# Optimization experiments

Measured on AMD Instinct MI355X. Metric: run time of the kernel, lower is better.

The kernel has to match this reference:

```python
import jax, jax.numpy as jnp
import numpy as np

H = 4        # no_heads
CH = 32      # per-head hidden (c_hidden)
INF = 1.0e9

def setup_inputs() -> dict:
    key = jax.random.key(0)
    ks = jax.random.split(key, 8)
    B, I, J, C = 1, 256, 256, 128
    s = 0.02
    return {
        "x": jax.random.normal(ks[0], (B, I, J, C), jnp.float32),
        "mask": jnp.ones((B, I, J), jnp.float32),
        "chunk_size": 0,
        "ln_w": jnp.ones((C,), jnp.float32),
        "ln_b": jnp.zeros((C,), jnp.float32),
        "w_tri": jax.random.normal(ks[1], (C, H), jnp.float32) * s,
        "wq": jax.random.normal(ks[2], (C, H * CH), jnp.float32) * s,
        "wk": jax.random.normal(ks[3], (C, H * CH), jnp.float32) * s,
        "wv": jax.random.normal(ks[4], (C, H * CH), jnp.float32) * s,
        "wg": jax.random.normal(ks[5], (C, H * CH), jnp.float32) * s,
        "bg": jnp.zeros((H * CH,), jnp.float32),
        "wo": jax.random.normal(ks[6], (H * CH, C), jnp.float32) * s,
        "bo": jnp.zeros((C,), jnp.float32),
    }

def _layer_norm(x, w, b, eps=1e-5):
    mu = jnp.mean(x, axis=-1, keepdims=True)
    var = jnp.mean(jnp.square(x - mu), axis=-1, keepdims=True)
    return (x - mu) * jax.lax.rsqrt(var + eps) * w + b

def reference(x, mask, chunk_size, ln_w, ln_b, w_tri, wq, wk, wv, wg, bg, wo, bo):
    # starting=True -> no transpose of (I, J)
    B, I, J, C = x.shape
    xn = _layer_norm(x, ln_w, ln_b)                                   # [B,I,J,C]
    # biases
    mask_bias = (INF * (mask - 1.0))[:, :, None, None, :]             # [B,I,1,1,J]
    tri_bias = jnp.einsum("bijc,ch->bhij", xn, w_tri)[:, None]        # [B,1,H,I,J]
    # gated multi-head attention over the J axis (per row I)
    q = (xn @ wq).reshape(B, I, J, H, CH) * (CH ** -0.5)              # [B,I,J,H,CH]
    k = (xn @ wk).reshape(B, I, J, H, CH)
    v = (xn @ wv).reshape(B, I, J, H, CH)
    scores = jnp.einsum("biqhd,bikhd->bihqk", q, k) + mask_bias + tri_bias
    a = jax.nn.softmax(scores, axis=-1)                               # [B,I,H,J,J]
    o = jnp.einsum("bihqk,bikhd->biqhd", a, v)                        # [B,I,J,H,CH]
    g = jax.nn.sigmoid(xn @ wg + bg).reshape(B, I, J, H, CH)
    o = (o * g).reshape(B, I, J, H * CH)
    return o @ wo + bo                                                # [B,I,J,C]
```

## Files before the change

kernel.cpp:

```cpp
#include <hip/hip_runtime.h>
#include <math.h>

#define NI 256
#define NJ 256
#define NC 128
#define NH 4
#define NCH 32
#define LOG2E 1.4426950408889634f

typedef _Float16 f16x8 __attribute__((ext_vector_type(8)));
typedef unsigned short u16x8 __attribute__((ext_vector_type(8)));
typedef unsigned int u32x4 __attribute__((ext_vector_type(4)));
typedef float f32x16 __attribute__((ext_vector_type(16)));

__device__ __forceinline__ unsigned short f2h(float f) {
    return __builtin_bit_cast(unsigned short, (_Float16)f);
}
__device__ __forceinline__ unsigned pkrtz(float a, float b) {
    return __builtin_bit_cast(unsigned, __builtin_amdgcn_cvt_pkrtz(a, b));
}
__device__ __forceinline__ f32x16 fzero16() {
    f32x16 z;
#pragma unroll
    for (int r = 0; r < 16; ++r) z[r] = 0.f;
    return z;
}
__device__ __forceinline__ f32x16 mfma16f(f16x8 a, f16x8 b, f32x16 c) {
    return __builtin_amdgcn_mfma_f32_32x32x16_f16(a, b, c, 0, 0, 0);
}

__global__ __launch_bounds__(256) void convert_weights(
    const float* __restrict__ wq, const float* __restrict__ wk,
    const float* __restrict__ wv, const float* __restrict__ wg,
    const float* __restrict__ wo, const float* __restrict__ w_tri,
    unsigned short* __restrict__ Wt_all, unsigned short* __restrict__ Wto,
    unsigned short* __restrict__ Wtri_pad)
{
    int id = blockIdx.x * 256 + threadIdx.x;
    if (id < 4 * 16384) {
        int m = id >> 14, r = id & 16383;
        int kk = r >> 7, c = r & 127;
        const float* W = (m == 0) ? wq : (m == 1) ? wk : (m == 2) ? wv : wg;
        Wt_all[(m * 128 + c) * 128 + kk] = f2h(W[kk * 128 + c]);
    } else if (id < 5 * 16384) {
        int r = id - 4 * 16384;
        int kk = r >> 7, c = r & 127;
        Wto[c * 128 + kk] = f2h(wo[kk * 128 + c]);
    } else {
        int r = id - 5 * 16384;
        int col = r >> 7, kk = r & 127;
        Wtri_pad[col * 128 + kk] = (col < NH) ? f2h(w_tri[kk * NH + col]) : (unsigned short)0;
    }
}

#define XNP 136
__global__ __launch_bounds__(256, 2) void ln_proj_mfma(
    const float* __restrict__ x, const float* __restrict__ ln_w, const float* __restrict__ ln_b,
    const unsigned short* __restrict__ Wt_all, const unsigned short* __restrict__ Wtri_pad,
    const float* __restrict__ bg,
    unsigned short* __restrict__ q, unsigned short* __restrict__ k,
    unsigned short* __restrict__ v, unsigned short* __restrict__ g,
    float* __restrict__ tri)
{
    __shared__ unsigned short xn[64 * XNP];
    const int tid = threadIdx.x;
    const long tok0 = (long)blockIdx.x * 64;

    const int lane8 = tid & 7;
#pragma unroll
    for (int p = 0; p < 2; ++p) {
        const int t = p * 32 + (tid >> 3);
        const float4* xrow = (const float4*)(x + (tok0 + t) * NC + lane8 * 16);
        float4 xv[4];
        float s = 0.f;
#pragma unroll
        for (int u = 0; u < 4; ++u) {
            xv[u] = xrow[u];
            s += xv[u].x + xv[u].y + xv[u].z + xv[u].w;
        }
#pragma unroll
        for (int off = 4; off; off >>= 1) s += __shfl_down(s, off, 8);
        const float mu = __shfl(s, 0, 8) * (1.f / (float)NC);
        float s2 = 0.f;
#pragma unroll
        for (int u = 0; u < 4; ++u) {
            float dx;
            dx = xv[u].x - mu; s2 += dx * dx;
            dx = xv[u].y - mu; s2 += dx * dx;
            dx = xv[u].z - mu; s2 += dx * dx;
            dx = xv[u].w - mu; s2 += dx * dx;
        }
#pragma unroll
        for (int off = 4; off; off >>= 1) s2 += __shfl_down(s2, off, 8);
        const float rstd = rsqrtf(__shfl(s2, 0, 8) * (1.f / (float)NC) + 1e-5f);
#pragma unroll
        for (int u = 0; u < 4; ++u) {
            const int c = lane8 * 16 + u * 4;
            const float4 lw = *(const float4*)(ln_w + c);
            const float4 lb = *(const float4*)(ln_b + c);
            float o0 = (xv[u].x - mu) * rstd * lw.x + lb.x;
            float o1 = (xv[u].y - mu) * rstd * lw.y + lb.y;
            float o2 = (xv[u].z - mu) * rstd * lw.z + lb.z;
            float o3 = (xv[u].w - mu) * rstd * lw.w + lb.w;
            *(unsigned*)&xn[t * XNP + c]     = pkrtz(o0, o1);
            *(unsigned*)&xn[t * XNP + c + 2] = pkrtz(o2, o3);
        }
    }
    __syncthreads();

    const int w = tid >> 6, L = tid & 63, lh = L >> 5, lc = L & 31;
    f32x16 acc[2][4], accT[2];
#pragma unroll
    for (int mt = 0; mt < 2; ++mt) {
        accT[mt] = fzero16();
#pragma unroll
        for (int nt = 0; nt < 4; ++nt) acc[mt][nt] = fzero16();
    }

#pragma unroll
    for (int k0 = 0; k0 < 8; ++k0) {
        f16x8 a0 = *(const f16x8*)&xn[(lc)      * XNP + k0 * 16 + lh * 8];
        f16x8 a1 = *(const f16x8*)&xn[(32 + lc) * XNP + k0 * 16 + lh * 8];
#pragma unroll
        for (int nt = 0; nt < 4; ++nt) {
            const int ntile = w + 4 * nt;
            f16x8 b = *(const f16x8*)&Wt_all[(ntile * 32 + lc) * 128 + k0 * 16 + lh * 8];
            acc[0][nt] = mfma16f(a0, b, acc[0][nt]);
            acc[1][nt] = mfma16f(a1, b, acc[1][nt]);
        }
        f16x8 bt = *(const f16x8*)&Wtri_pad[lc * 128 + k0 * 16 + lh * 8];
        accT[0] = mfma16f(a0, bt, accT[0]);
        accT[1] = mfma16f(a1, bt, accT[1]);
    }

    const int a_row = (int)(tok0 >> 8);
    const int b0    = (int)(tok0 & 255);
    int rowl[16];
#pragma unroll
    for (int r = 0; r < 16; ++r) rowl[r] = (r & 3) + 8 * (r >> 2) + 4 * lh;

    if (lc < NH) {
        float* tb = tri + ((long)lc * NI + a_row) * NJ + b0;
#pragma unroll
        for (int mt = 0; mt < 2; ++mt)
#pragma unroll
            for (int r = 0; r < 16; ++r)
                tb[mt * 32 + rowl[r]] = accT[mt][r];
    }

    const float bgv = bg[w * 32 + lc];
    const int token = tid >> 2, c8 = (tid & 3) * 8;
#pragma unroll
    for (int m = 0; m < 4; ++m) {
        __syncthreads();
#pragma unroll
        for (int mt = 0; mt < 2; ++mt) {
#pragma unroll
            for (int r = 0; r < 16; ++r) {
                const int row = mt * 32 + rowl[r];
                float val = acc[mt][m][r];
                if (m == 0) val *= 0.25503486f;
                if (m == 3) val = __builtin_amdgcn_rcpf(1.f + __builtin_amdgcn_exp2f(-LOG2E * (val + bgv)));
                xn[row * XNP + w * 32 + lc] = f2h(val);
            }
        }
        __syncthreads();
        unsigned short* O = (m == 0) ? q : (m == 1) ? k : (m == 2) ? v : g;
#pragma unroll
        for (int hh = 0; hh < 4; ++hh) {
            const u16x8 vec = *(const u16x8*)&xn[token * XNP + hh * 32 + c8];
            *(u16x8*)(O + (((long)a_row * NH + hh) * NJ + b0 + token) * NCH + c8) = vec;
        }
    }
}

__global__ __launch_bounds__(64) void swizzle_triT(
    const float* __restrict__ tri, float* __restrict__ tswz)
{
    __shared__ float Ls[32 * 36];
    const int h = blockIdx.x, qt = blockIdx.y, kt = blockIdx.z;
    const int l = threadIdx.x;
#pragma unroll
    for (int rr = 0; rr < 4; ++rr) {
        const int fi = rr * 64 + l;
        const int row = fi >> 3, c4 = fi & 7;
        *(float4*)&Ls[row * 36 + c4 * 4] =
            *(const float4*)(tri + ((long)h * NI + qt * 32 + row) * NJ + kt * 32 + c4 * 4);
    }
    __syncthreads();
    const int lc = l & 31, lhh = l >> 5;
    float* dst = tswz + (((long)(h * 8 + qt) * 8 + kt) * 64 + l) * 16;
    float vals[16];
#pragma unroll
    for (int r = 0; r < 16; ++r)
        vals[r] = LOG2E * Ls[lc * 36 + kt * 0 + (r & 3) + 8 * (r >> 2) + 4 * lhh];
#pragma unroll
    for (int u = 0; u < 4; ++u)
        *(float4*)(dst + u * 4) = make_float4(vals[4*u], vals[4*u+1], vals[4*u+2], vals[4*u+3]);
}

#define KSP 40
#define VTP 264
#define QSP 40
#define GSP 40
__global__ __launch_bounds__(512, 4) void attn_fused(
    const unsigned short* __restrict__ q, const unsigned short* __restrict__ k,
    const unsigned short* __restrict__ v, const unsigned short* __restrict__ g,
    const float* __restrict__ tswz, const float* __restrict__ mask,
    const unsigned short* __restrict__ Wto, const float* __restrict__ bo,
    float* __restrict__ out)
{
    __shared__ char smem[79360];
    unsigned short* Ks = (unsigned short*)(smem);
    unsigned short* Vt = (unsigned short*)(smem + 20480);
    unsigned short* Qs = (unsigned short*)(smem + 37376);
    unsigned short* Gs = (unsigned short*)(smem + 47616);
    float*       maskb = (float*)(smem + 57856);
    float*         mrg = (float*)(smem + 58880);

    const int i = blockIdx.x, qh = blockIdx.y;
    const int tid = threadIdx.x;
    const int w = tid >> 6, L = tid & 63, lh = L >> 5, lc = L & 31;
    const int wq4 = w & 3, ku = w >> 2;
    const int qt = qh * 4 + wq4;
    const int tb0 = ku * 4;

    if (tid < 256) maskb[tid] = (LOG2E * 1.0e9f) * (mask[i * NJ + tid] - 1.0f);

    int rowl[16];
#pragma unroll
    for (int r = 0; r < 16; ++r) rowl[r] = (r & 3) + 8 * (r >> 2) + 4 * lh;

    f32x16 outacc[2];
    outacc[0] = fzero16(); outacc[1] = fzero16();
    float* myMrg = mrg + ((long)wq4 * 64 + L) * 20;

    for (int h = 0; h < NH; ++h) {
        const long base = ((long)i * NH + h) * NJ * NCH;
#pragma unroll
        for (int it = 0; it < 2; ++it) {
            const int idx = it * 512 + tid;
            const int key = idx >> 2, c8 = (idx & 3) * 8;
            *(u16x8*)&Ks[key * KSP + c8] = *(const u16x8*)(k + base + key * NCH + c8);
        }
        {
            const int row = tid >> 2, c8 = (tid & 3) * 8;
            *(u16x8*)&Qs[row * QSP + c8] = *(const u16x8*)(q + base + (qh * 128 + row) * NCH + c8);
            *(u16x8*)&Gs[row * GSP + c8] = *(const u16x8*)(g + base + (qh * 128 + row) * NCH + c8);
        }
        {
            const int key = tid >> 1, hf = tid & 1;
            const u16x8 r0 = *(const u16x8*)(v + base + key * NCH + hf * 16);
            const u16x8 r1 = *(const u16x8*)(v + base + key * NCH + hf * 16 + 8);
#pragma unroll
            for (int u = 0; u < 8; ++u) {
                Vt[(hf * 16 + u)     * VTP + key] = r0[u];
                Vt[(hf * 16 + 8 + u) * VTP + key] = r1[u];
            }
        }
        __syncthreads();

        const f16x8 a0 = *(const f16x8*)&Qs[(wq4 * 32 + lc) * QSP + lh * 8];
        const f16x8 a1 = *(const f16x8*)&Qs[(wq4 * 32 + lc) * QSP + 16 + lh * 8];

        float ls = 0.f;
        f32x16 O = fzero16();

#pragma unroll
        for (int tt = 0; tt < 4; ++tt) {
            const int t = tb0 + tt;
            const float* tv = tswz + (((long)(h * 8 + qt)) * 8 + t) * 1024 + (long)L * 16;
            f32x16 s;
#pragma unroll
            for (int u = 0; u < 4; ++u) {
                const float4 t4 = *(const float4*)(tv + u * 4);
                s[4*u] = t4.x; s[4*u+1] = t4.y; s[4*u+2] = t4.z; s[4*u+3] = t4.w;
            }
            const f16x8 kb0 = *(const f16x8*)&Ks[(t * 32 + lc) * KSP + lh * 8];
            const f16x8 kb1 = *(const f16x8*)&Ks[(t * 32 + lc) * KSP + 16 + lh * 8];
            s = mfma16f(kb0, a0, s);
            s = mfma16f(kb1, a1, s);

            unsigned pk[8];
#pragma unroll
            for (int gg = 0; gg < 4; ++gg) {
                const float4 mb = *(const float4*)&maskb[t * 32 + gg * 8 + 4 * lh];
                const float p0 = __builtin_amdgcn_exp2f(fminf(s[4*gg+0] + mb.x, 15.f));
                const float p1 = __builtin_amdgcn_exp2f(fminf(s[4*gg+1] + mb.y, 15.f));
                const float p2 = __builtin_amdgcn_exp2f(fminf(s[4*gg+2] + mb.z, 15.f));
                const float p3 = __builtin_amdgcn_exp2f(fminf(s[4*gg+3] + mb.w, 15.f));
                ls += (p0 + p1) + (p2 + p3);
                pk[2*gg]   = pkrtz(p0, p1);
                pk[2*gg+1] = pkrtz(p2, p3);
            }
#pragma unroll
            for (int ss = 0; ss < 2; ++ss) {
                const unsigned give0 = lh ? pk[4*ss]   : pk[4*ss+2];
                const unsigned give1 = lh ? pk[4*ss+1] : pk[4*ss+3];
                const unsigned t0 = __shfl_xor(give0, 32);
                const unsigned t1 = __shfl_xor(give1, 32);
                u32x4 bw;
                bw[0] = lh ? t0 : pk[4*ss];
                bw[1] = lh ? t1 : pk[4*ss+1];
                bw[2] = lh ? pk[4*ss+2] : t0;
                bw[3] = lh ? pk[4*ss+3] : t1;
                const f16x8 pb = __builtin_bit_cast(f16x8, bw);
                const f16x8 va = *(const f16x8*)&Vt[lc * VTP + t * 32 + ss * 16 + lh * 8];
                O = mfma16f(va, pb, O);
            }
        }

        if (ku) {
#pragma unroll
            for (int u = 0; u < 4; ++u)
                *(float4*)(myMrg + u * 4) = make_float4(O[4*u], O[4*u+1], O[4*u+2], O[4*u+3]);
            myMrg[16] = ls;
        }
        __syncthreads();
        if (!ku) {
#pragma unroll
            for (int u = 0; u < 4; ++u) {
                const float4 p4 = *(const float4*)(myMrg + u * 4);
                O[4*u] += p4.x; O[4*u+1] += p4.y; O[4*u+2] += p4.z; O[4*u+3] += p4.w;
            }
            ls += myMrg[16];
            ls += __shfl_xor(ls, 32);
            const float rl = __builtin_amdgcn_rcpf(ls);
            unsigned pg[8];
#pragma unroll
            for (int gg = 0; gg < 4; ++gg) {
                const unsigned short* gp = &Gs[(wq4 * 32 + lc) * GSP + gg * 8 + 4 * lh];
                const float o0 = O[4*gg+0] * rl * (float)*(const _Float16*)&gp[0];
                const float o1 = O[4*gg+1] * rl * (float)*(const _Float16*)&gp[1];
                const float o2 = O[4*gg+2] * rl * (float)*(const _Float16*)&gp[2];
                const float o3 = O[4*gg+3] * rl * (float)*(const _Float16*)&gp[3];
                pg[2*gg]   = pkrtz(o0, o1);
                pg[2*gg+1] = pkrtz(o2, o3);
            }
            unsigned obw[8];
#pragma unroll
            for (int ss = 0; ss < 2; ++ss) {
                const unsigned give0 = lh ? pg[4*ss]   : pg[4*ss+2];
                const unsigned give1 = lh ? pg[4*ss+1] : pg[4*ss+3];
                const unsigned t0 = __shfl_xor(give0, 32);
                const unsigned t1 = __shfl_xor(give1, 32);
                obw[4*ss+0] = lh ? t0 : pg[4*ss];
                obw[4*ss+1] = lh ? t1 : pg[4*ss+1];
                obw[4*ss+2] = lh ? pg[4*ss+2] : t0;
                obw[4*ss+3] = lh ? pg[4*ss+3] : t1;
            }
            u32x4 w0, w1;
#pragma unroll
            for (int u = 0; u < 4; ++u) { w0[u] = obw[u]; w1[u] = obw[4+u]; }
            ((u32x4*)myMrg)[0] = w0;
            ((u32x4*)myMrg)[1] = w1;
        }
        __syncthreads();
        {
            const u32x4 b0v = ((const u32x4*)myMrg)[0];
            const u32x4 b1v = ((const u32x4*)myMrg)[1];
#pragma unroll
            for (int ss = 0; ss < 2; ++ss) {
                const f16x8 ogf = __builtin_bit_cast(f16x8, ss ? b1v : b0v);
#pragma unroll
                for (int c2 = 0; c2 < 2; ++c2) {
                    const f16x8 wa = *(const f16x8*)(Wto + ((ku * 2 + c2) * 32 + lc) * NC
                                                     + h * NCH + ss * 16 + lh * 8);
                    outacc[c2] = mfma16f(wa, ogf, outacc[c2]);
                }
            }
        }
    }

    float* outs = (float*)smem;
#pragma unroll
    for (int ph = 0; ph < 2; ++ph) {
        __syncthreads();
        if (ku == ph) {
#pragma unroll
            for (int c2 = 0; c2 < 2; ++c2)
#pragma unroll
                for (int r = 0; r < 16; ++r)
                    outs[(wq4 * 32 + lc) * 68 + c2 * 32 + rowl[r]] = outacc[c2][r];
        }
        __syncthreads();
#pragma unroll
        for (int it = 0; it < 4; ++it) {
            const int fi = it * 512 + tid;
            const int qrow = fi >> 4, c4 = fi & 15;
            const float4 vv = *(const float4*)&outs[qrow * 68 + c4 * 4];
            const float4 b4 = *(const float4*)(bo + ph * 64 + c4 * 4);
            float4 st;
            st.x = vv.x + b4.x; st.y = vv.y + b4.y;
            st.z = vv.z + b4.z; st.w = vv.w + b4.w;
            *(float4*)(out + ((long)i * NJ + qh * 128 + qrow) * NC + ph * 64 + c4 * 4) = st;
        }
    }
}

extern "C" void kernel_launch(void* const* d_in, const int* in_sizes, int n_in,
                              void* d_out, int out_size, void* d_ws, size_t ws_size,
                              hipStream_t stream) {
    const float* x     = (const float*)d_in[0];
    const float* mask  = (const float*)d_in[1];
    const float* ln_w  = (const float*)d_in[3];
    const float* ln_b  = (const float*)d_in[4];
    const float* w_tri = (const float*)d_in[5];
    const float* wq    = (const float*)d_in[6];
    const float* wk    = (const float*)d_in[7];
    const float* wv    = (const float*)d_in[8];
    const float* wg    = (const float*)d_in[9];
    const float* bg    = (const float*)d_in[10];
    const float* wo    = (const float*)d_in[11];
    const float* bo    = (const float*)d_in[12];
    float* out = (float*)d_out;

    char* p = (char*)d_ws;
    const long TOK = (long)NI * NJ;
    const long QB  = TOK * NC * sizeof(unsigned short);
    unsigned short* q  = (unsigned short*)p; p += QB;
    unsigned short* k  = (unsigned short*)p; p += QB;
    unsigned short* v  = (unsigned short*)p; p += QB;
    unsigned short* g  = (unsigned short*)p; p += QB;
    float* tri  = (float*)p; p += (long)NH * NI * NJ * sizeof(float);
    float* tswz = (float*)p; p += (long)NH * NI * NJ * sizeof(float);
    unsigned short* Wt_all   = (unsigned short*)p; p += 4 * 128 * 128 * sizeof(unsigned short);
    unsigned short* Wto      = (unsigned short*)p; p += 128 * 128 * sizeof(unsigned short);
    unsigned short* Wtri_pad = (unsigned short*)p; p += 32 * 128 * sizeof(unsigned short);

    hipLaunchKernelGGL(convert_weights, dim3(336), dim3(256), 0, stream,
                       wq, wk, wv, wg, wo, w_tri, Wt_all, Wto, Wtri_pad);
    hipLaunchKernelGGL(ln_proj_mfma, dim3(TOK / 64), dim3(256), 0, stream,
                       x, ln_w, ln_b, Wt_all, Wtri_pad, bg, q, k, v, g, tri);
    hipLaunchKernelGGL(swizzle_triT, dim3(NH, 8, 8), dim3(64), 0, stream, tri, tswz);
    hipLaunchKernelGGL(attn_fused, dim3(NI, 2), dim3(512), 0, stream,
                       q, k, v, g, tswz, mask, Wto, bo, out);
}
```

Baseline: 181.4 us.

## Store Q/K/V in MFMA fragment layout and drop attention LDS staging

The projection kernel now writes Q, K and V directly in the per-lane MFMA fragment order, 32-token tiles per head, with V pre-transposed. The attention kernel can then load its operands straight from global memory instead of staging K, V^T and Q through shared memory, which removes the LDS transposes and cuts shared memory enough to raise occupancy. The projection kernel moves to 32-token blocks with per-wave transpose buffers, and weight conversion uses tiled LDS transposes. In exchange, K/V fragments are re-read from global/L2 by every wave rather than shared through LDS.

```diff
diff --git a/kernel.cpp b/kernel.cpp
--- a/kernel.cpp
+++ b/kernel.cpp
@@ -36,40 +36,47 @@
     unsigned short* __restrict__ Wt_all, unsigned short* __restrict__ Wto,
     unsigned short* __restrict__ Wtri_pad)
 {
-    int id = blockIdx.x * 256 + threadIdx.x;
-    if (id < 4 * 16384) {
-        int m = id >> 14, r = id & 16383;
-        int kk = r >> 7, c = r & 127;
-        const float* W = (m == 0) ? wq : (m == 1) ? wk : (m == 2) ? wv : wg;
-        Wt_all[(m * 128 + c) * 128 + kk] = f2h(W[kk * 128 + c]);
-    } else if (id < 5 * 16384) {
-        int r = id - 4 * 16384;
-        int kk = r >> 7, c = r & 127;
-        Wto[c * 128 + kk] = f2h(wo[kk * 128 + c]);
+    __shared__ float Ls[32][33];
+    const int b = blockIdx.x;
+    const int tid = threadIdx.x;
+    if (b < 80) {
+        const int m = b >> 4, tile = b & 15, tr = tile >> 2, tc = tile & 3;
+        const float* W = (m == 0) ? wq : (m == 1) ? wk : (m == 2) ? wv : (m == 3) ? wg : wo;
+        const int r = tid >> 3, c4 = (tid & 7) * 4;
+        const float4 v4 = *(const float4*)(W + (tr * 32 + r) * 128 + tc * 32 + c4);
+        Ls[r][c4 + 0] = v4.x; Ls[r][c4 + 1] = v4.y;
+        Ls[r][c4 + 2] = v4.z; Ls[r][c4 + 3] = v4.w;
+        __syncthreads();
+        unsigned short* D = (m < 4) ? (Wt_all + m * 16384) : Wto;
+        ushort4 o;
+        o.x = f2h(Ls[c4 + 0][r]); o.y = f2h(Ls[c4 + 1][r]);
+        o.z = f2h(Ls[c4 + 2][r]); o.w = f2h(Ls[c4 + 3][r]);
+        *(ushort4*)(D + (tc * 32 + r) * 128 + tr * 32 + c4) = o;
     } else {
-        int r = id - 5 * 16384;
-        int col = r >> 7, kk = r & 127;
-        Wtri_pad[col * 128 + kk] = (col < NH) ? f2h(w_tri[kk * NH + col]) : (unsigned short)0;
+        const int kk = tid & 127, c0 = tid >> 7;
+        for (int cc = c0; cc < 32; cc += 2)
+            Wtri_pad[cc * 128 + kk] = (cc < NH) ? f2h(w_tri[kk * NH + cc]) : (unsigned short)0;
     }
 }
 
 #define XNP 136
-__global__ __launch_bounds__(256, 2) void ln_proj_mfma(
+#define TSP 40
+__global__ __launch_bounds__(256, 3) void ln_proj_mfma(
     const float* __restrict__ x, const float* __restrict__ ln_w, const float* __restrict__ ln_b,
     const unsigned short* __restrict__ Wt_all, const unsigned short* __restrict__ Wtri_pad,
     const float* __restrict__ bg,
-    unsigned short* __restrict__ q, unsigned short* __restrict__ k,
-    unsigned short* __restrict__ v, unsigned short* __restrict__ g,
+    unsigned short* __restrict__ q_f, unsigned short* __restrict__ k_f,
+    unsigned short* __restrict__ v_f, unsigned short* __restrict__ g_p,
     float* __restrict__ tri)
 {
-    __shared__ unsigned short xn[64 * XNP];
+    __shared__ unsigned short xn[32 * XNP];
+    __shared__ unsigned short tw[4][32 * TSP];
     const int tid = threadIdx.x;
-    const long tok0 = (long)blockIdx.x * 64;
+    const long tok0 = (long)blockIdx.x * 32;
 
     const int lane8 = tid & 7;
-#pragma unroll
-    for (int p = 0; p < 2; ++p) {
-        const int t = p * 32 + (tid >> 3);
+    const int t = tid >> 3;
+    {
         const float4* xrow = (const float4*)(x + (tok0 + t) * NC + lane8 * 16);
         float4 xv[4];
         float s = 0.f;
@@ -109,67 +116,64 @@
     __syncthreads();
 
     const int w = tid >> 6, L = tid & 63, lh = L >> 5, lc = L & 31;
-    f32x16 acc[2][4], accT[2];
-#pragma unroll
-    for (int mt = 0; mt < 2; ++mt) {
-        accT[mt] = fzero16();
-#pragma unroll
-        for (int nt = 0; nt < 4; ++nt) acc[mt][nt] = fzero16();
-    }
+    f32x16 acc[4], accT;
+#pragma unroll
+    for (int nt = 0; nt < 4; ++nt) acc[nt] = fzero16();
+    accT = fzero16();
 
 #pragma unroll
     for (int k0 = 0; k0 < 8; ++k0) {
-        f16x8 a0 = *(const f16x8*)&xn[(lc)      * XNP + k0 * 16 + lh * 8];
-        f16x8 a1 = *(const f16x8*)&xn[(32 + lc) * XNP + k0 * 16 + lh * 8];
+        const f16x8 a0 = *(const f16x8*)&xn[lc * XNP + k0 * 16 + lh * 8];
 #pragma unroll
         for (int nt = 0; nt < 4; ++nt) {
-            const int ntile = w + 4 * nt;
-            f16x8 b = *(const f16x8*)&Wt_all[(ntile * 32 + lc) * 128 + k0 * 16 + lh * 8];
-            acc[0][nt] = mfma16f(a0, b, acc[0][nt]);
-            acc[1][nt] = mfma16f(a1, b, acc[1][nt]);
-        }
-        f16x8 bt = *(const f16x8*)&Wtri_pad[lc * 128 + k0 * 16 + lh * 8];
-        accT[0] = mfma16f(a0, bt, accT[0]);
-        accT[1] = mfma16f(a1, bt, accT[1]);
-    }
-
-    const int a_row = (int)(tok0 >> 8);
-    const int b0    = (int)(tok0 & 255);
+            const f16x8 b = *(const f16x8*)&Wt_all[((w + 4 * nt) * 32 + lc) * 128 + k0 * 16 + lh * 8];
+            acc[nt] = mfma16f(a0, b, acc[nt]);
+        }
+        if (w == 0) {
+            const f16x8 bt = *(const f16x8*)&Wtri_pad[lc * 128 + k0 * 16 + lh * 8];
+            accT = mfma16f(a0, bt, accT);
+        }
+    }
+
+    const int i_row = (int)(tok0 >> 8), j0 = (int)(tok0 & 255), tloc = j0 >> 5;
     int rowl[16];
 #pragma unroll
     for (int r = 0; r < 16; ++r) rowl[r] = (r & 3) + 8 * (r >> 2) + 4 * lh;
 
-    if (lc < NH) {
-        float* tb = tri + ((long)lc * NI + a_row) * NJ + b0;
-#pragma unroll
-        for (int mt = 0; mt < 2; ++mt)
-#pragma unroll
-            for (int r = 0; r < 16; ++r)
-                tb[mt * 32 + rowl[r]] = accT[mt][r];
+    if (w == 0 && lc < NH) {
+        float* tb = tri + ((long)lc * NI + i_row) * NJ + j0;
+#pragma unroll
+        for (int r = 0; r < 16; ++r) tb[rowl[r]] = accT[r];
     }
 
     const float bgv = bg[w * 32 + lc];
-    const int token = tid >> 2, c8 = (tid & 3) * 8;
+    unsigned short* T = tw[w];
 #pragma unroll
     for (int m = 0; m < 4; ++m) {
-        __syncthreads();
-#pragma unroll
-        for (int mt = 0; mt < 2; ++mt) {
-#pragma unroll
-            for (int r = 0; r < 16; ++r) {
-                const int row = mt * 32 + rowl[r];
-                float val = acc[mt][m][r];
-                if (m == 0) val *= 0.25503486f;
-                if (m == 3) val = __builtin_amdgcn_rcpf(1.f + __builtin_amdgcn_exp2f(-LOG2E * (val + bgv)));
-                xn[row * XNP + w * 32 + lc] = f2h(val);
-            }
-        }
-        __syncthreads();
-        unsigned short* O = (m == 0) ? q : (m == 1) ? k : (m == 2) ? v : g;
-#pragma unroll
-        for (int hh = 0; hh < 4; ++hh) {
-            const u16x8 vec = *(const u16x8*)&xn[token * XNP + hh * 32 + c8];
-            *(u16x8*)(O + (((long)a_row * NH + hh) * NJ + b0 + token) * NCH + c8) = vec;
+#pragma unroll
+        for (int r = 0; r < 16; ++r) {
+            float val = acc[m][r];
+            if (m == 0) val *= 0.25503486f;
+            if (m == 3) val = __builtin_amdgcn_rcpf(1.f + __builtin_amdgcn_exp2f(-LOG2E * (val + bgv)));
+            if (m == 2) T[lc * TSP + rowl[r]] = f2h(val);
+            else        T[rowl[r] * TSP + lc] = f2h(val);
+        }
+        if (m == 3) {
+#pragma unroll
+            for (int it = 0; it < 2; ++it) {
+                const int u = it * 64 + L;
+                const int tk = u >> 2, c8 = (u & 3) * 8;
+                const u16x8 vec = *(const u16x8*)&T[tk * TSP + c8];
+                *(u16x8*)(g_p + (((long)i_row * NH + w) * NJ + j0 + tk) * NCH + c8) = vec;
+            }
+        } else {
+            unsigned short* dst = ((m == 0) ? q_f : (m == 1) ? k_f : v_f)
+                                  + (((long)i_row * NH + w) * 8 + tloc) * 1024;
+#pragma unroll
+            for (int ss = 0; ss < 2; ++ss) {
+                const u16x8 vec = *(const u16x8*)&T[lc * TSP + ss * 16 + lh * 8];
+                *(u16x8*)(dst + ss * 512 + L * 8) = vec;
+            }
         }
     }
 }
@@ -193,30 +197,26 @@
     float vals[16];
 #pragma unroll
     for (int r = 0; r < 16; ++r)
-        vals[r] = LOG2E * Ls[lc * 36 + kt * 0 + (r & 3) + 8 * (r >> 2) + 4 * lhh];
+        vals[r] = LOG2E * Ls[lc * 36 + (r & 3) + 8 * (r >> 2) + 4 * lhh];
 #pragma unroll
     for (int u = 0; u < 4; ++u)
         *(float4*)(dst + u * 4) = make_float4(vals[4*u], vals[4*u+1], vals[4*u+2], vals[4*u+3]);
 }
 
-#define KSP 40
-#define VTP 264
-#define QSP 40
 #define GSP 40
-__global__ __launch_bounds__(512, 4) void attn_fused(
-    const unsigned short* __restrict__ q, const unsigned short* __restrict__ k,
-    const unsigned short* __restrict__ v, const unsigned short* __restrict__ g,
+#define MRGS 20
+__global__ __launch_bounds__(512, 6) void attn_fused(
+    const unsigned short* __restrict__ q_f, const unsigned short* __restrict__ k_f,
+    const unsigned short* __restrict__ v_f, const unsigned short* __restrict__ g_p,
     const float* __restrict__ tswz, const float* __restrict__ mask,
     const unsigned short* __restrict__ Wto, const float* __restrict__ bo,
     float* __restrict__ out)
 {
-    __shared__ char smem[79360];
-    unsigned short* Ks = (unsigned short*)(smem);
-    unsigned short* Vt = (unsigned short*)(smem + 20480);
-    unsigned short* Qs = (unsigned short*)(smem + 37376);
-    unsigned short* Gs = (unsigned short*)(smem + 47616);
-    float*       maskb = (float*)(smem + 57856);
-    float*         mrg = (float*)(smem + 58880);
+    __shared__ char smem[34816];
+    unsigned short* Gs = (unsigned short*)smem;
+    float* maskb = (float*)(smem + 10240);
+    float* mrg   = (float*)(smem + 11264);
+    float* outs  = (float*)smem;
 
     const int i = blockIdx.x, qh = blockIdx.y;
     const int tid = threadIdx.x;
@@ -233,35 +233,20 @@
 
     f32x16 outacc[2];
     outacc[0] = fzero16(); outacc[1] = fzero16();
-    float* myMrg = mrg + ((long)wq4 * 64 + L) * 20;
+    float* myO = mrg + ((long)(wq4 * 64) + L) * MRGS;
 
     for (int h = 0; h < NH; ++h) {
-        const long base = ((long)i * NH + h) * NJ * NCH;
-#pragma unroll
-        for (int it = 0; it < 2; ++it) {
-            const int idx = it * 512 + tid;
-            const int key = idx >> 2, c8 = (idx & 3) * 8;
-            *(u16x8*)&Ks[key * KSP + c8] = *(const u16x8*)(k + base + key * NCH + c8);
-        }
+        if (h) __syncthreads();
+        const long fb = ((long)i * NH + h) * 8;
         {
             const int row = tid >> 2, c8 = (tid & 3) * 8;
-            *(u16x8*)&Qs[row * QSP + c8] = *(const u16x8*)(q + base + (qh * 128 + row) * NCH + c8);
-            *(u16x8*)&Gs[row * GSP + c8] = *(const u16x8*)(g + base + (qh * 128 + row) * NCH + c8);
-        }
-        {
-            const int key = tid >> 1, hf = tid & 1;
-            const u16x8 r0 = *(const u16x8*)(v + base + key * NCH + hf * 16);
-            const u16x8 r1 = *(const u16x8*)(v + base + key * NCH + hf * 16 + 8);
-#pragma unroll
-            for (int u = 0; u < 8; ++u) {
-                Vt[(hf * 16 + u)     * VTP + key] = r0[u];
-                Vt[(hf * 16 + 8 + u) * VTP + key] = r1[u];
-            }
-        }
-        __syncthreads();
-
-        const f16x8 a0 = *(const f16x8*)&Qs[(wq4 * 32 + lc) * QSP + lh * 8];
-        const f16x8 a1 = *(const f16x8*)&Qs[(wq4 * 32 + lc) * QSP + 16 + lh * 8];
+            *(u16x8*)&Gs[row * GSP + c8] =
+                *(const u16x8*)(g_p + (((long)i * NH + h) * NJ + qh * 128 + row) * NCH + c8);
+        }
+        __syncthreads();
+
+        const f16x8 a0 = *(const f16x8*)(q_f + (fb + qt) * 1024 + L * 8);
+        const f16x8 a1 = *(const f16x8*)(q_f + (fb + qt) * 1024 + 512 + L * 8);
 
         float ls = 0.f;
         f32x16 O = fzero16();
@@ -276,8 +261,8 @@
                 const float4 t4 = *(const float4*)(tv + u * 4);
                 s[4*u] = t4.x; s[4*u+1] = t4.y; s[4*u+2] = t4.z; s[4*u+3] = t4.w;
             }
-            const f16x8 kb0 = *(const f16x8*)&Ks[(t * 32 + lc) * KSP + lh * 8];
-            const f16x8 kb1 = *(const f16x8*)&Ks[(t * 32 + lc) * KSP + 16 + lh * 8];
+            const f16x8 kb0 = *(const f16x8*)(k_f + (fb + t) * 1024 + L * 8);
+            const f16x8 kb1 = *(const f16x8*)(k_f + (fb + t) * 1024 + 512 + L * 8);
             s = mfma16f(kb0, a0, s);
             s = mfma16f(kb1, a1, s);
 
@@ -305,7 +290,7 @@
                 bw[2] = lh ? pk[4*ss+2] : t0;
                 bw[3] = lh ? pk[4*ss+3] : t1;
                 const f16x8 pb = __builtin_bit_cast(f16x8, bw);
-                const f16x8 va = *(const f16x8*)&Vt[lc * VTP + t * 32 + ss * 16 + lh * 8];
+                const f16x8 va = *(const f16x8*)(v_f + (fb + t) * 1024 + ss * 512 + L * 8);
                 O = mfma16f(va, pb, O);
             }
         }
@@ -313,17 +298,17 @@
         if (ku) {
 #pragma unroll
             for (int u = 0; u < 4; ++u)
-                *(float4*)(myMrg + u * 4) = make_float4(O[4*u], O[4*u+1], O[4*u+2], O[4*u+3]);
-            myMrg[16] = ls;
+                *(float4*)(myO + u * 4) = make_float4(O[4*u], O[4*u+1], O[4*u+2], O[4*u+3]);
+            myO[16] = ls;
         }
         __syncthreads();
         if (!ku) {
 #pragma unroll
             for (int u = 0; u < 4; ++u) {
-                const float4 p4 = *(const float4*)(myMrg + u * 4);
+                const float4 p4 = *(const float4*)(myO + u * 4);
                 O[4*u] += p4.x; O[4*u+1] += p4.y; O[4*u+2] += p4.z; O[4*u+3] += p4.w;
             }
-            ls += myMrg[16];
+            ls += myO[16];
             ls += __shfl_xor(ls, 32);
             const float rl = __builtin_amdgcn_rcpf(ls);
             unsigned pg[8];
@@ -352,13 +337,13 @@
             u32x4 w0, w1;
 #pragma unroll
             for (int u = 0; u < 4; ++u) { w0[u] = obw[u]; w1[u] = obw[4+u]; }
-            ((u32x4*)myMrg)[0] = w0;
-            ((u32x4*)myMrg)[1] = w1;
+            ((u32x4*)myO)[0] = w0;
+            ((u32x4*)myO)[1] = w1;
         }
         __syncthreads();
         {
-            const u32x4 b0v = ((const u32x4*)myMrg)[0];
-            const u32x4 b1v = ((const u32x4*)myMrg)[1];
+            const u32x4 b0v = ((const u32x4*)myO)[0];
+            const u32x4 b1v = ((const u32x4*)myO)[1];
 #pragma unroll
             for (int ss = 0; ss < 2; ++ss) {
                 const f16x8 ogf = __builtin_bit_cast(f16x8, ss ? b1v : b0v);
@@ -372,7 +357,6 @@
         }
     }
 
-    float* outs = (float*)smem;
 #pragma unroll
     for (int ph = 0; ph < 2; ++ph) {
         __syncthreads();
@@ -418,21 +402,21 @@
     char* p = (char*)d_ws;
     const long TOK = (long)NI * NJ;
     const long QB  = TOK * NC * sizeof(unsigned short);
-    unsigned short* q  = (unsigned short*)p; p += QB;
-    unsigned short* k  = (unsigned short*)p; p += QB;
-    unsigned short* v  = (unsigned short*)p; p += QB;
-    unsigned short* g  = (unsigned short*)p; p += QB;
+    unsigned short* q_f = (unsigned short*)p; p += QB;
+    unsigned short* k_f = (unsigned short*)p; p += QB;
+    unsigned short* v_f = (unsigned short*)p; p += QB;
+    unsigned short* g_p = (unsigned short*)p; p += QB;
     float* tri  = (float*)p; p += (long)NH * NI * NJ * sizeof(float);
     float* tswz = (float*)p; p += (long)NH * NI * NJ * sizeof(float);
     unsigned short* Wt_all   = (unsigned short*)p; p += 4 * 128 * 128 * sizeof(unsigned short);
     unsigned short* Wto      = (unsigned short*)p; p += 128 * 128 * sizeof(unsigned short);
     unsigned short* Wtri_pad = (unsigned short*)p; p += 32 * 128 * sizeof(unsigned short);
 
-    hipLaunchKernelGGL(convert_weights, dim3(336), dim3(256), 0, stream,
+    hipLaunchKernelGGL(convert_weights, dim3(81), dim3(256), 0, stream,
                        wq, wk, wv, wg, wo, w_tri, Wt_all, Wto, Wtri_pad);
-    hipLaunchKernelGGL(ln_proj_mfma, dim3(TOK / 64), dim3(256), 0, stream,
-                       x, ln_w, ln_b, Wt_all, Wtri_pad, bg, q, k, v, g, tri);
+    hipLaunchKernelGGL(ln_proj_mfma, dim3(TOK / 32), dim3(256), 0, stream,
+                       x, ln_w, ln_b, Wt_all, Wtri_pad, bg, q_f, k_f, v_f, g_p, tri);
     hipLaunchKernelGGL(swizzle_triT, dim3(NH, 8, 8), dim3(64), 0, stream, tri, tswz);
     hipLaunchKernelGGL(attn_fused, dim3(NI, 2), dim3(512), 0, stream,
-                       q, k, v, g, tswz, mask, Wto, bo, out);
-}
+                       q_f, k_f, v_f, g_p, tswz, mask, Wto, bo, out);
+}
```

Measured after the change: 220.4 us. 1.21x slower.
